# Performance work log

Hardware: AMD Instinct MI355X
Metric: run time of the kernel (lower is better)

The kernel has to match this reference:

```python
import jax, jax.numpy as jnp
from jax import lax
import numpy as np

B, DIM, H, W = 1, 48, 192, 192
HEADS, K, DIL = 2, 7, 3
HD = DIM // HEADS
HID = int(DIM * 2.66)  # 127 (Restormer GEGLU hidden)
EPS = 1e-5


def _window_starts(L, Kk, D):
    # NATTEN window-start rule: keep phase i % D, shift window inside bounds.
    s = np.zeros(L, dtype=np.int32)
    for i in range(L):
        if D <= 1:
            st = max(i - Kk // 2, 0)
            if i + Kk // 2 >= L:
                st = L - Kk
        else:
            st = i - (Kk // 2) * D
            if st < 0:
                st = i % D
            elif i + (Kk // 2) * D >= L:
                imodd = i % D
                a = (L // D) * D
                b = L - a
                if imodd < b:
                    st = L - b + imodd - 2 * (Kk // 2) * D
                else:
                    st = a + imodd - Kk * D
        s[i] = st
    return s


def _nbr_tables(L, Kk, D):
    st = _window_starts(L, Kk, D)
    idx = st[:, None] + np.arange(Kk)[None, :] * D          # [L, K] absolute neighbor idx
    pb = (st - np.arange(L)) // D                            # signed offset of window start (in dilation units)
    pb = pb[:, None] + (Kk - 1) + np.arange(Kk)[None, :]     # [L, K] rpb index in [0, 2K-2]
    return jnp.asarray(idx), jnp.asarray(pb)

IH, PBH = _nbr_tables(H, K, DIL)
IW, PBW = _nbr_tables(W, K, DIL)


def layernorm(x, w, b):  # channel LN on NCHW (WithBias, biased var)
    mu = x.mean(1, keepdims=True)
    var = ((x - mu) ** 2).mean(1, keepdims=True)
    return (x - mu) / jnp.sqrt(var + EPS) * w[None, :, None, None] + b[None, :, None, None]


def na2d(x, qkv_w, qkv_b, rpb, proj_w, proj_b):
    # x: NCHW -> BHWC
    t = x.transpose(0, 2, 3, 1)
    qkv = t @ qkv_w.T + qkv_b                                # [B,H,W,3*DIM]
    qkv = qkv.reshape(B, H, W, 3, HEADS, HD)
    q, k, v = qkv[:, :, :, 0], qkv[:, :, :, 1], qkv[:, :, :, 2]
    q = q * (HD ** -0.5)
    # gather dilated 7x7 neighborhoods: [B, H, K, W, K, heads, hd]
    kn = k[:, IH[:, :, None, None], IW[None, None, :, :]]
    vn = v[:, IH[:, :, None, None], IW[None, None, :, :]]
    attn = jnp.einsum('bijnc,bixjync->bijnxy', q, kn)        # [B,H,W,heads,K,K]
    bias = rpb[:, PBH][:, :, :, PBW]                         # [heads,H,K,W,K]
    attn = attn + bias.transpose(1, 3, 0, 2, 4)
    attn = jax.nn.softmax(attn.reshape(B, H, W, HEADS, K * K), axis=-1)
    attn = attn.reshape(B, H, W, HEADS, K, K)
    out = jnp.einsum('bijnxy,bixjync->bijnc', attn, vn).reshape(B, H, W, DIM)
    out = out @ proj_w.T + proj_b
    return out.transpose(0, 3, 1, 2)


def chan_mod(x, eca_w):  # ECA-style gate: GAP -> 1D conv over channels -> sigmoid
    p = x.mean((2, 3))                                       # [B,C]
    y = lax.conv_general_dilated(p[:, None, :], eca_w[None, None, :], (1,), [(3, 3)],
                                 dimension_numbers=('NCH', 'OIH', 'NCH'))[:, 0, :]
    return jax.nn.sigmoid(y)[:, :, None, None]


def ffn(x, w_in, w_dw, w_out):  # conv-GEGLU
    t = jnp.einsum('bchw,oc->bohw', x, w_in)                 # 1x1: DIM -> 2*HID
    t = lax.conv_general_dilated(t, w_dw, (1, 1), [(1, 1), (1, 1)],
                                 feature_group_count=2 * HID,
                                 dimension_numbers=('NCHW', 'OIHW', 'NCHW'))
    x1, x2 = t[:, :HID], t[:, HID:]
    g = jax.nn.gelu(x1, approximate=False) * x2
    return jnp.einsum('bchw,oc->bohw', g, w_out)             # 1x1: HID -> DIM


def setup_inputs() -> dict:
    key = jax.random.key(0)
    ks = jax.random.split(key, 10)
    d = {
        'x': jax.random.normal(ks[0], (B, DIM, H, W), jnp.float32),
        'ln1_w': jnp.ones((DIM,), jnp.float32),
        'ln1_b': jnp.zeros((DIM,), jnp.float32),
        'qkv_w': jax.random.normal(ks[1], (3 * DIM, DIM), jnp.float32) * 0.05,
        'qkv_b': jnp.zeros((3 * DIM,), jnp.float32),
        'rpb': jax.random.normal(ks[2], (HEADS, 2 * K - 1, 2 * K - 1), jnp.float32) * 0.02,
        'proj_w': jax.random.normal(ks[3], (DIM, DIM), jnp.float32) * 0.05,
        'proj_b': jnp.zeros((DIM,), jnp.float32),
        'eca_w': jax.random.normal(ks[4], (7,), jnp.float32) * 0.1,
        'ln2_w': jnp.ones((DIM,), jnp.float32),
        'ln2_b': jnp.zeros((DIM,), jnp.float32),
        'w_in': jax.random.normal(ks[5], (2 * HID, DIM), jnp.float32) * 0.05,
        'w_dw': jax.random.normal(ks[6], (2 * HID, 1, 3, 3), jnp.float32) * 0.05,
        'w_out': jax.random.normal(ks[7], (DIM, HID), jnp.float32) * 0.05,
    }
    return d


def reference(x, ln1_w, ln1_b, qkv_w, qkv_b, rpb, proj_w, proj_b, eca_w,
              ln2_w, ln2_b, w_in, w_dw, w_out):
    xn1 = layernorm(x, ln1_w, ln1_b)
    x = x + na2d(xn1, qkv_w, qkv_b, rpb, proj_w, proj_b) * chan_mod(xn1, eca_w)
    x = x + ffn(layernorm(x, ln2_w, ln2_b), w_in, w_dw, w_out)
    return x
```

## Files before the change

kernel.cpp:

```cpp
#include <hip/hip_runtime.h>
#include <hip/hip_bf16.h>
#include <math.h>

#define HW_ (192*192)
#define Wd 192
#define HIDc 127
#define NBLK1 (HW_/64)

#define O_LN1W 0
#define O_QKVW 96
#define O_QKVB 7008
#define O_RPB  7152
#define O_PROJW 7490
#define O_PROJB 9794
#define O_ECA  9842
#define O_LN2W 9849
#define O_WIN  9945
#define O_WDW  22137
#define O_WOUT 24423
#define WTS_LEN 30519

typedef unsigned short ushort_t;

__device__ __forceinline__ float b2f(__hip_bfloat16 v){ return __bfloat162float(v); }
__device__ __forceinline__ float u2f(ushort_t h){ return __uint_as_float(((unsigned)h)<<16); }
__device__ __forceinline__ ushort_t f2u(float f){
    __hip_bfloat16 h = __float2bfloat16(f);
    union { __hip_bfloat16 b; ushort_t u; } c; c.b = h; return c.u;
}
__device__ __forceinline__ void up2(unsigned u, float& a, float& b){
    a = __uint_as_float(u << 16);
    b = __uint_as_float(u & 0xffff0000u);
}

__device__ __forceinline__ int wstart(int i){
    if (i < 9) return i % 3;
    if (i >= 183) return 171 + (i % 3);
    return i - 9;
}

__global__ void convert_kernel(
    const void* p0, const void* p1, const void* p2, const void* p3,
    const void* p4, const void* p5, const void* p6, const void* p7,
    const void* p8, const void* p9, const void* p10, const void* p11,
    const void* p12, const ushort_t* __restrict__ xu, int* __restrict__ mode_out,
    float* __restrict__ wts, ushort_t* __restrict__ qkvbf, float* __restrict__ woutT)
{
    __shared__ int sbad;
    if (threadIdx.x == 0) sbad = 0;
    __syncthreads();
    {
        unsigned u = xu[2*threadIdx.x];
        float f = __uint_as_float(u << 16);
        if (!(fabsf(f) < 100.f)) atomicAdd(&sbad, 1);
    }
    __syncthreads();
    const int md = (sbad > 16) ? 1 : 0;
    if (blockIdx.x == 0 && threadIdx.x == 0) mode_out[0] = md;

    const void* ps[13] = {p0,p1,p2,p3,p4,p5,p6,p7,p8,p9,p10,p11,p12};
    const int sz[13]  = {48,48,6912,144,338,2304,48,7,48,48,12192,2286,6096};
    const int off[13] = {O_LN1W,48,O_QKVW,O_QKVB,O_RPB,O_PROJW,O_PROJB,O_ECA,
                         O_LN2W,9897,O_WIN,O_WDW,O_WOUT};
    int b = blockIdx.x;
    if (b == 13){
        if (md){
            const float* s = (const float*)p2;
            for (int i = threadIdx.x; i < 6912; i += 256) qkvbf[i] = f2u(s[i]);
        } else {
            const ushort_t* s = (const ushort_t*)p2;
            for (int i = threadIdx.x; i < 6912; i += 256) qkvbf[i] = s[i];
        }
        return;
    }
    if (b == 14){
        if (md){
            const float* s = (const float*)p12;
            for (int i = threadIdx.x; i < 6096; i += 256){
                int c = i / 48, o = i - c*48;
                woutT[i] = s[o*127 + c];
            }
        } else {
            const __hip_bfloat16* s = (const __hip_bfloat16*)p12;
            for (int i = threadIdx.x; i < 6096; i += 256){
                int c = i / 48, o = i - c*48;
                woutT[i] = b2f(s[o*127 + c]);
            }
        }
        return;
    }
    int n = sz[b];
    float* dst = wts + off[b];
    if (md){
        const float* s = (const float*)ps[b];
        for (int i = threadIdx.x; i < n; i += 256) dst[i] = s[i];
    } else {
        const __hip_bfloat16* s = (const __hip_bfloat16*)ps[b];
        for (int i = threadIdx.x; i < n; i += 256) dst[i] = b2f(s[i]);
    }
}

__global__ __launch_bounds__(384) void ln1qkv_kernel(
    const void* __restrict__ x, const int* __restrict__ mode,
    const float* __restrict__ wts, const ushort_t* __restrict__ qkvbf,
    ushort_t* __restrict__ q, ushort_t* __restrict__ k, ushort_t* __restrict__ v,
    float* __restrict__ chpart)
{
    __shared__ float sx[64*49];

    const int tid  = threadIdx.x;
    const int px_l = tid & 63;
    const int r6   = __builtin_amdgcn_readfirstlane(tid >> 6);
    const int p0   = blockIdx.x * 64;
    const int p    = p0 + px_l;

    if (mode[0]){
        const float* xf = (const float*)x;
        for (int idx = tid; idx < 64*48; idx += 384){
            int c = idx >> 6, pl = idx & 63;
            sx[pl*49 + c] = xf[c*HW_ + p0 + pl];
        }
    } else {
        const __hip_bfloat16* xb = (const __hip_bfloat16*)x;
        for (int idx = tid; idx < 64*48; idx += 384){
            int c = idx >> 6, pl = idx & 63;
            sx[pl*49 + c] = b2f(xb[c*HW_ + p0 + pl]);
        }
    }
    __syncthreads();

    float xr[48];
    float mu = 0.f;
    #pragma unroll
    for (int c = 0; c < 48; c++){ xr[c] = sx[px_l*49 + c]; mu += xr[c]; }
    mu *= (1.f/48.f);
    float var = 0.f;
    #pragma unroll
    for (int c = 0; c < 48; c++){ float d = xr[c]-mu; var += d*d; }
    var *= (1.f/48.f);
    float rs = rsqrtf(var + 1e-5f);
    #pragma unroll
    for (int c = 0; c < 48; c++)
        xr[c] = (xr[c]-mu)*rs*wts[O_LN1W + c] + wts[O_LN1W + 48 + c];

    if (tid < 64){
        #pragma unroll
        for (int c = 0; c < 48; c++){
            float s = xr[c];
            s += __shfl_xor(s, 1);  s += __shfl_xor(s, 2);  s += __shfl_xor(s, 4);
            s += __shfl_xor(s, 8);  s += __shfl_xor(s, 16); s += __shfl_xor(s, 32);
            if (tid == 0) chpart[blockIdx.x*48 + c] = s;
        }
    }

    const int rbase = r6 * 24;
    const float scale = (r6 < 2) ? 0.20412414523193154f : 1.0f;
    float ov[24];
    #pragma unroll 4
    for (int ro = 0; ro < 24; ro++){
        int r = rbase + ro;
        float acc = wts[O_QKVB + r];
        const uint4* wr = (const uint4*)(qkvbf + r*48);
        #pragma unroll
        for (int c8 = 0; c8 < 6; c8++){
            uint4 u = wr[c8];
            float f0,f1,f2,f3,f4,f5,f6,f7;
            up2(u.x,f0,f1); up2(u.y,f2,f3); up2(u.z,f4,f5); up2(u.w,f6,f7);
            acc += f0*xr[8*c8]   + f1*xr[8*c8+1] + f2*xr[8*c8+2] + f3*xr[8*c8+3]
                 + f4*xr[8*c8+4] + f5*xr[8*c8+5] + f6*xr[8*c8+6] + f7*xr[8*c8+7];
        }
        ov[ro] = acc * scale;
    }

    unsigned int pk[12];
    #pragma unroll
    for (int d = 0; d < 12; d++)
        pk[d] = (unsigned)f2u(ov[2*d]) | ((unsigned)f2u(ov[2*d+1]) << 16);
    ushort_t* tp = (r6 >> 1) == 0 ? q : ((r6 >> 1) == 1 ? k : v);
    uint4* dst4 = (uint4*)(tp + (size_t)p*48 + (r6 & 1)*24);
    dst4[0] = make_uint4(pk[0], pk[1], pk[2],  pk[3]);
    dst4[1] = make_uint4(pk[4], pk[5], pk[6],  pk[7]);
    dst4[2] = make_uint4(pk[8], pk[9], pk[10], pk[11]);
}

__global__ __launch_bounds__(256) void gatered_kernel(
    const float* __restrict__ chpart, float* __restrict__ msum)
{
    __shared__ float red[4];
    const int c = blockIdx.x;
    const int tid = threadIdx.x;
    float acc = 0.f;
    for (int b = tid; b < NBLK1; b += 256)
        acc += chpart[b*48 + c];
    acc += __shfl_xor(acc, 1);  acc += __shfl_xor(acc, 2);  acc += __shfl_xor(acc, 4);
    acc += __shfl_xor(acc, 8);  acc += __shfl_xor(acc, 16); acc += __shfl_xor(acc, 32);
    if ((tid & 63) == 0) red[tid >> 6] = acc;
    __syncthreads();
    if (tid == 0)
        msum[c] = (red[0] + red[1] + red[2] + red[3]) * (1.f / (float)HW_);
}

__global__ void gate_kernel(const float* __restrict__ msum,
                            const float* __restrict__ wts,
                            float* __restrict__ gate)
{
    __shared__ float m[48];
    int t = threadIdx.x;
    if (t < 48) m[t] = msum[t];
    __syncthreads();
    if (t < 48){
        float a = 0.f;
        for (int kk = 0; kk < 7; kk++){
            int cc = t + kk - 3;
            if (cc >= 0 && cc < 48) a += wts[O_ECA + kk] * m[cc];
        }
        gate[t] = 1.f / (1.f + expf(-a));
    }
}

__global__ __launch_bounds__(256) void attn_kernel(
    const ushort_t* __restrict__ q, const ushort_t* __restrict__ k,
    const ushort_t* __restrict__ v, const float* __restrict__ wts,
    ushort_t* __restrict__ aout)
{
    const int head = blockIdx.y;
    __shared__ float srpb[169];
    for (int i = threadIdx.x; i < 169; i += 256) srpb[i] = wts[O_RPB + head*169 + i];
    __syncthreads();

    const int tid  = threadIdx.x;
    const int px   = blockIdx.x * 128 + (tid >> 1);
    const int half = tid & 1;
    const int i = px / Wd, j = px % Wd;
    const int sti = wstart(i), stj = wstart(j);
    const int pbi = (sti - i) / 3 + 6;
    const int pbj = (stj - j) / 3 + 6;
    const int choff = head*24 + half*12;

    float qr[12];
    {
        const ushort4* qp = (const ushort4*)(q + (size_t)px*48 + choff);
        #pragma unroll
        for (int b = 0; b < 3; b++){
            ushort4 uu = qp[b];
            qr[4*b]   = u2f(uu.x); qr[4*b+1] = u2f(uu.y);
            qr[4*b+2] = u2f(uu.z); qr[4*b+3] = u2f(uu.w);
        }
    }

    float m = -1e30f, s = 0.f;
    float acc[12];
    #pragma unroll
    for (int c = 0; c < 12; c++) acc[c] = 0.f;

    #pragma unroll
    for (int xx = 0; xx < 7; xx++){
        int ii = sti + 3*xx;
        #pragma unroll
        for (int yy = 0; yy < 7; yy++){
            int jj = stj + 3*yy;
            const size_t nb = (size_t)(ii*Wd + jj)*48 + choff;
            const ushort4* kp = (const ushort4*)(k + nb);
            const ushort4* vp = (const ushort4*)(v + nb);
            ushort4 k0 = kp[0], k1 = kp[1], k2 = kp[2];
            ushort4 v0 = vp[0], v1 = vp[1], v2 = vp[2];
            float d = qr[0]*u2f(k0.x) + qr[1]*u2f(k0.y)
                    + qr[2]*u2f(k0.z) + qr[3]*u2f(k0.w)
                    + qr[4]*u2f(k1.x) + qr[5]*u2f(k1.y)
                    + qr[6]*u2f(k1.z) + qr[7]*u2f(k1.w)
                    + qr[8]*u2f(k2.x) + qr[9]*u2f(k2.y)
                    + qr[10]*u2f(k2.z) + qr[11]*u2f(k2.w);
            d += __shfl_xor(d, 1);
            float sc = d + srpb[(pbi+xx)*13 + (pbj+yy)];
            float mn = fmaxf(m, sc);
            float corr = __expf(m - mn);
            float p = __expf(sc - mn);
            s = s*corr + p;
            m = mn;
            acc[0]  = acc[0] *corr + p*u2f(v0.x);
            acc[1]  = acc[1] *corr + p*u2f(v0.y);
            acc[2]  = acc[2] *corr + p*u2f(v0.z);
            acc[3]  = acc[3] *corr + p*u2f(v0.w);
            acc[4]  = acc[4] *corr + p*u2f(v1.x);
            acc[5]  = acc[5] *corr + p*u2f(v1.y);
            acc[6]  = acc[6] *corr + p*u2f(v1.z);
            acc[7]  = acc[7] *corr + p*u2f(v1.w);
            acc[8]  = acc[8] *corr + p*u2f(v2.x);
            acc[9]  = acc[9] *corr + p*u2f(v2.y);
            acc[10] = acc[10]*corr + p*u2f(v2.z);
            acc[11] = acc[11]*corr + p*u2f(v2.w);
        }
    }
    const float inv = 1.f / s;
    #pragma unroll
    for (int c = 0; c < 12; c++)
        aout[(size_t)(choff + c)*HW_ + px] = f2u(acc[c] * inv);
}

__global__ __launch_bounds__(512) void projpw1_kernel(
    const ushort_t* __restrict__ aout, const float* __restrict__ wts,
    const float* __restrict__ gate, const void* __restrict__ x,
    const int* __restrict__ mode, float* __restrict__ x2,
    ushort_t* __restrict__ t)
{
    __shared__ float saout[64*49];
    __shared__ float sx2[64*49];

    const int tid  = threadIdx.x;
    const int px_l = tid & 63;
    const int og   = __builtin_amdgcn_readfirstlane(tid >> 6);
    const int px0  = blockIdx.x * 64;
    const int px   = px0 + px_l;

    for (int idx = tid; idx < 64*48; idx += 512){
        int c = idx >> 6, pl = idx & 63;
        saout[pl*49 + c] = u2f(aout[(size_t)c*HW_ + px0 + pl]);
    }
    __syncthreads();

    float ar[48];
    #pragma unroll
    for (int c = 0; c < 48; c++) ar[c] = saout[px_l*49 + c];

    const float* xf = (const float*)x;
    const __hip_bfloat16* xb = (const __hip_bfloat16*)x;
    const int md = mode[0];
    const int ob = og * 6;
    #pragma unroll
    for (int oo = 0; oo < 6; oo++){
        int o = ob + oo;
        float acc = wts[O_PROJB + o];
        const float4* swr = (const float4*)&wts[O_PROJW + o*48];
        #pragma unroll
        for (int c4 = 0; c4 < 12; c4++){
            float4 w = swr[c4];
            acc += w.x*ar[4*c4] + w.y*ar[4*c4+1] + w.z*ar[4*c4+2] + w.w*ar[4*c4+3];
        }
        float res = md ? xf[o*HW_ + px] : b2f(xb[o*HW_ + px]);
        float val = res + acc * gate[o];
        x2[o*HW_ + px] = val;
        sx2[px_l*49 + o] = val;
    }
    __syncthreads();

    float xr[48];
    float mu = 0.f;
    #pragma unroll
    for (int c = 0; c < 48; c++){ xr[c] = sx2[px_l*49 + c]; mu += xr[c]; }
    mu *= (1.f/48.f);
    float var = 0.f;
    #pragma unroll
    for (int c = 0; c < 48; c++){ float d = xr[c]-mu; var += d*d; }
    var *= (1.f/48.f);
    float rs = rsqrtf(var + 1e-5f);
    #pragma unroll
    for (int c = 0; c < 48; c++)
        xr[c] = (xr[c]-mu)*rs*wts[O_LN2W + c] + wts[O_LN2W + 48 + c];

    const int o20 = og * 32;
    #pragma unroll 2
    for (int t2 = 0; t2 < 32; t2++){
        int o2 = o20 + t2;
        if (o2 >= 254) break;
        float acc = 0.f;
        const float4* swr = (const float4*)&wts[O_WIN + o2*48];
        #pragma unroll
        for (int c4 = 0; c4 < 12; c4++){
            float4 w = swr[c4];
            acc += w.x*xr[4*c4] + w.y*xr[4*c4+1] + w.z*xr[4*c4+2] + w.w*xr[4*c4+3];
        }
        t[(size_t)o2*HW_ + px] = f2u(acc);
    }
}

__global__ __launch_bounds__(256) void dw_kernel(
    const ushort_t* __restrict__ t, const float* __restrict__ wts,
    ushort_t* __restrict__ g)
{
    int ch = blockIdx.y;
    int p  = blockIdx.x * 256 + threadIdx.x;
    int i  = p / Wd, j = p % Wd;
    float w1[9], w2[9];
    #pragma unroll
    for (int s = 0; s < 9; s++){
        w1[s] = wts[O_WDW + ch*9 + s];
        w2[s] = wts[O_WDW + (ch+HIDc)*9 + s];
    }
    const ushort_t* t1 = t + (size_t)ch * HW_;
    const ushort_t* t2 = t + (size_t)(ch+HIDc) * HW_;
    float a1 = 0.f, a2 = 0.f;
    #pragma unroll
    for (int di = 0; di < 3; di++){
        int ii = i + di - 1;
        if (ii < 0 || ii >= 192) continue;
        #pragma unroll
        for (int dj = 0; dj < 3; dj++){
            int jj = j + dj - 1;
            if (jj < 0 || jj >= 192) continue;
            int off = ii*Wd + jj;
            a1 += w1[di*3+dj]*u2f(t1[off]);
            a2 += w2[di*3+dj]*u2f(t2[off]);
        }
    }
    float ge = a1 * 0.5f * (1.f + erff(a1 * 0.70710678118654752f));
    g[(size_t)ch*HW_ + p] = f2u(ge * a2);
}

__global__ __launch_bounds__(128) void pw2_kernel(
    const ushort_t* __restrict__ g, const float* __restrict__ woutT,
    const float* __restrict__ x2, void* __restrict__ outv,
    const int* __restrict__ mode)
{
    const int ob = blockIdx.y * 12;
    const int p  = blockIdx.x * 128 + threadIdx.x;
    float acc[12];
    #pragma unroll
    for (int o = 0; o < 12; o++) acc[o] = 0.f;
    #pragma unroll 4
    for (int c = 0; c < 127; c++){
        float gv = u2f(g[(size_t)c*HW_ + p]);
        const float* wr = woutT + c*48 + ob;
        #pragma unroll
        for (int o = 0; o < 12; o++) acc[o] += wr[o]*gv;
    }
    if (mode[0]){
        float* out = (float*)outv;
        #pragma unroll
        for (int o = 0; o < 12; o++){
            int oc = ob + o;
            out[(size_t)oc*HW_ + p] = x2[(size_t)oc*HW_ + p] + acc[o];
        }
    } else {
        __hip_bfloat16* out = (__hip_bfloat16*)outv;
        #pragma unroll
        for (int o = 0; o < 12; o++){
            int oc = ob + o;
            out[(size_t)oc*HW_ + p] =
                __float2bfloat16(x2[(size_t)oc*HW_ + p] + acc[o]);
        }
    }
}

extern "C" void kernel_launch(void* const* d_in, const int* in_sizes, int n_in,
                              void* d_out, int out_size, void* d_ws, size_t ws_size,
                              hipStream_t stream)
{
    (void)in_sizes; (void)n_in; (void)out_size;

    char* ws = (char*)d_ws;
    ushort_t* q    = (ushort_t*)(ws);
    ushort_t* k    = (ushort_t*)(ws + 3538944);
    ushort_t* v    = (ushort_t*)(ws + 7077888);
    ushort_t* aout = (ushort_t*)(ws + 10616832);
    ushort_t* t    = (ushort_t*)(ws);
    float*    x2   = (float*)   (ws + 18726912);
    ushort_t* g    = (ushort_t*)(ws + 25804800);
    float*    gate = (float*)   (ws + 35168448);
    int*      mode = (int*)     (ws + 35168640);
    float*    wts  = (float*)   (ws + 35168656);
    float*    chpart=(float*)   (ws + 35168656 + (size_t)WTS_LEN*4);
    float*    msum = chpart + (size_t)NBLK1*48;
    ushort_t* qkvbf= (ushort_t*)(msum + 48);
    float*    woutT= (float*)(qkvbf + 6912);

    size_t need = 35168656 + (size_t)WTS_LEN*4 + (size_t)NBLK1*48*4 + 48*4
                + 6912*2 + 6096*4;
    if (ws_size < need) return;

    convert_kernel<<<15, 256, 0, stream>>>(
        d_in[1], d_in[2], d_in[3], d_in[4], d_in[5], d_in[6], d_in[7],
        d_in[8], d_in[9], d_in[10], d_in[11], d_in[12], d_in[13],
        (const ushort_t*)d_in[0], mode, wts, qkvbf, woutT);

    ln1qkv_kernel<<<dim3(NBLK1), 384, 0, stream>>>(d_in[0], mode, wts, qkvbf,
                                                   q, k, v, chpart);
    gatered_kernel<<<48, 256, 0, stream>>>(chpart, msum);
    gate_kernel<<<1, 64, 0, stream>>>(msum, wts, gate);
    attn_kernel<<<dim3(HW_/128, 2), 256, 0, stream>>>(q, k, v, wts, aout);
    projpw1_kernel<<<dim3(HW_/64), 512, 0, stream>>>(aout, wts, gate, d_in[0],
                                                     mode, x2, t);
    dw_kernel<<<dim3(HW_/256, 127), 256, 0, stream>>>(t, wts, g);
    pw2_kernel<<<dim3(HW_/128, 4), 128, 0, stream>>>(g, woutT, x2, d_out, mode);
}
```

Baseline: 279.9 us.

## Use bf16 proj/w_in weights and halve projpw1 block size with more outputs per thread

The convert kernel now also produces bf16 copies of the projection and GEGLU input weights. projpw1 reads them with 16-byte packed loads, and each thread now computes 12 proj outputs and 64 pw1 outputs, two rows at a time. The block shrinks from 512 to 256 threads and the shared-memory transpose of aout is dropped in favour of direct coalesced per-channel loads. The aim is fewer weight-load instructions and less LDS traffic, at the cost of more serial work per thread and lower weight precision.

```diff
diff --git a/kernel.cpp b/kernel.cpp
--- a/kernel.cpp
+++ b/kernel.cpp
@@ -39,12 +39,26 @@
     return i - 9;
 }
 
+__device__ __forceinline__ float dot48bf(const uint4* wr, const float* xr){
+    float acc = 0.f;
+    #pragma unroll
+    for (int c8 = 0; c8 < 6; c8++){
+        uint4 u = wr[c8];
+        float f0,f1,f2,f3,f4,f5,f6,f7;
+        up2(u.x,f0,f1); up2(u.y,f2,f3); up2(u.z,f4,f5); up2(u.w,f6,f7);
+        acc += f0*xr[8*c8]   + f1*xr[8*c8+1] + f2*xr[8*c8+2] + f3*xr[8*c8+3]
+             + f4*xr[8*c8+4] + f5*xr[8*c8+5] + f6*xr[8*c8+6] + f7*xr[8*c8+7];
+    }
+    return acc;
+}
+
 __global__ void convert_kernel(
     const void* p0, const void* p1, const void* p2, const void* p3,
     const void* p4, const void* p5, const void* p6, const void* p7,
     const void* p8, const void* p9, const void* p10, const void* p11,
     const void* p12, const ushort_t* __restrict__ xu, int* __restrict__ mode_out,
-    float* __restrict__ wts, ushort_t* __restrict__ qkvbf, float* __restrict__ woutT)
+    float* __restrict__ wts, ushort_t* __restrict__ qkvbf, float* __restrict__ woutT,
+    ushort_t* __restrict__ winbf, ushort_t* __restrict__ projbf)
 {
     __shared__ int sbad;
     if (threadIdx.x == 0) sbad = 0;
@@ -63,28 +77,44 @@
     const int off[13] = {O_LN1W,48,O_QKVW,O_QKVB,O_RPB,O_PROJW,O_PROJB,O_ECA,
                          O_LN2W,9897,O_WIN,O_WDW,O_WOUT};
     int b = blockIdx.x;
-    if (b == 13){
-        if (md){
-            const float* s = (const float*)p2;
-            for (int i = threadIdx.x; i < 6912; i += 256) qkvbf[i] = f2u(s[i]);
-        } else {
-            const ushort_t* s = (const ushort_t*)p2;
-            for (int i = threadIdx.x; i < 6912; i += 256) qkvbf[i] = s[i];
-        }
-        return;
-    }
-    if (b == 14){
-        if (md){
-            const float* s = (const float*)p12;
-            for (int i = threadIdx.x; i < 6096; i += 256){
-                int c = i / 48, o = i - c*48;
-                woutT[i] = s[o*127 + c];
+    if (b >= 13){
+        if (b == 13){
+            if (md){
+                const float* s = (const float*)p2;
+                for (int i = threadIdx.x; i < 6912; i += 256) qkvbf[i] = f2u(s[i]);
+            } else {
+                const ushort_t* s = (const ushort_t*)p2;
+                for (int i = threadIdx.x; i < 6912; i += 256) qkvbf[i] = s[i];
+            }
+        } else if (b == 14){
+            if (md){
+                const float* s = (const float*)p12;
+                for (int i = threadIdx.x; i < 6096; i += 256){
+                    int c = i / 48, o = i - c*48;
+                    woutT[i] = s[o*127 + c];
+                }
+            } else {
+                const __hip_bfloat16* s = (const __hip_bfloat16*)p12;
+                for (int i = threadIdx.x; i < 6096; i += 256){
+                    int c = i / 48, o = i - c*48;
+                    woutT[i] = b2f(s[o*127 + c]);
+                }
+            }
+        } else if (b == 15){
+            if (md){
+                const float* s = (const float*)p10;
+                for (int i = threadIdx.x; i < 12192; i += 256) winbf[i] = f2u(s[i]);
+            } else {
+                const ushort_t* s = (const ushort_t*)p10;
+                for (int i = threadIdx.x; i < 12192; i += 256) winbf[i] = s[i];
             }
         } else {
-            const __hip_bfloat16* s = (const __hip_bfloat16*)p12;
-            for (int i = threadIdx.x; i < 6096; i += 256){
-                int c = i / 48, o = i - c*48;
-                woutT[i] = b2f(s[o*127 + c]);
+            if (md){
+                const float* s = (const float*)p5;
+                for (int i = threadIdx.x; i < 2304; i += 256) projbf[i] = f2u(s[i]);
+            } else {
+                const ushort_t* s = (const ushort_t*)p5;
+                for (int i = threadIdx.x; i < 2304; i += 256) projbf[i] = s[i];
             }
         }
         return;
@@ -159,16 +189,8 @@
     #pragma unroll 4
     for (int ro = 0; ro < 24; ro++){
         int r = rbase + ro;
-        float acc = wts[O_QKVB + r];
-        const uint4* wr = (const uint4*)(qkvbf + r*48);
-        #pragma unroll
-        for (int c8 = 0; c8 < 6; c8++){
-            uint4 u = wr[c8];
-            float f0,f1,f2,f3,f4,f5,f6,f7;
-            up2(u.x,f0,f1); up2(u.y,f2,f3); up2(u.z,f4,f5); up2(u.w,f6,f7);
-            acc += f0*xr[8*c8]   + f1*xr[8*c8+1] + f2*xr[8*c8+2] + f3*xr[8*c8+3]
-                 + f4*xr[8*c8+4] + f5*xr[8*c8+5] + f6*xr[8*c8+6] + f7*xr[8*c8+7];
-        }
+        float acc = wts[O_QKVB + r]
+                  + dot48bf((const uint4*)(qkvbf + r*48), xr);
         ov[ro] = acc * scale;
     }
 
@@ -297,13 +319,13 @@
         aout[(size_t)(choff + c)*HW_ + px] = f2u(acc[c] * inv);
 }
 
-__global__ __launch_bounds__(512) void projpw1_kernel(
+__global__ __launch_bounds__(256) void projpw1_kernel(
     const ushort_t* __restrict__ aout, const float* __restrict__ wts,
+    const ushort_t* __restrict__ projbf, const ushort_t* __restrict__ winbf,
     const float* __restrict__ gate, const void* __restrict__ x,
     const int* __restrict__ mode, float* __restrict__ x2,
     ushort_t* __restrict__ t)
 {
-    __shared__ float saout[64*49];
     __shared__ float sx2[64*49];
 
     const int tid  = threadIdx.x;
@@ -312,30 +334,19 @@
     const int px0  = blockIdx.x * 64;
     const int px   = px0 + px_l;
 
-    for (int idx = tid; idx < 64*48; idx += 512){
-        int c = idx >> 6, pl = idx & 63;
-        saout[pl*49 + c] = u2f(aout[(size_t)c*HW_ + px0 + pl]);
-    }
-    __syncthreads();
-
     float ar[48];
     #pragma unroll
-    for (int c = 0; c < 48; c++) ar[c] = saout[px_l*49 + c];
+    for (int c = 0; c < 48; c++) ar[c] = u2f(aout[(size_t)c*HW_ + px]);
 
     const float* xf = (const float*)x;
     const __hip_bfloat16* xb = (const __hip_bfloat16*)x;
     const int md = mode[0];
-    const int ob = og * 6;
-    #pragma unroll
-    for (int oo = 0; oo < 6; oo++){
+    const int ob = og * 12;
+    #pragma unroll 2
+    for (int oo = 0; oo < 12; oo++){
         int o = ob + oo;
-        float acc = wts[O_PROJB + o];
-        const float4* swr = (const float4*)&wts[O_PROJW + o*48];
-        #pragma unroll
-        for (int c4 = 0; c4 < 12; c4++){
-            float4 w = swr[c4];
-            acc += w.x*ar[4*c4] + w.y*ar[4*c4+1] + w.z*ar[4*c4+2] + w.w*ar[4*c4+3];
-        }
+        float acc = wts[O_PROJB + o]
+                  + dot48bf((const uint4*)(projbf + o*48), ar);
         float res = md ? xf[o*HW_ + px] : b2f(xb[o*HW_ + px]);
         float val = res + acc * gate[o];
         x2[o*HW_ + px] = val;
@@ -357,19 +368,27 @@
     for (int c = 0; c < 48; c++)
         xr[c] = (xr[c]-mu)*rs*wts[O_LN2W + c] + wts[O_LN2W + 48 + c];
 
-    const int o20 = og * 32;
-    #pragma unroll 2
-    for (int t2 = 0; t2 < 32; t2++){
-        int o2 = o20 + t2;
-        if (o2 >= 254) break;
-        float acc = 0.f;
-        const float4* swr = (const float4*)&wts[O_WIN + o2*48];
-        #pragma unroll
-        for (int c4 = 0; c4 < 12; c4++){
-            float4 w = swr[c4];
-            acc += w.x*xr[4*c4] + w.y*xr[4*c4+1] + w.z*xr[4*c4+2] + w.w*xr[4*c4+3];
-        }
-        t[(size_t)o2*HW_ + px] = f2u(acc);
+    const int o20 = og * 64;
+    for (int t2 = 0; t2 < 64; t2 += 2){
+        int oA = o20 + t2;
+        if (oA >= 254) break;
+        const uint4* wA = (const uint4*)(winbf + oA*48);
+        const uint4* wB = (const uint4*)(winbf + (oA+1)*48);
+        float accA = 0.f, accB = 0.f;
+        #pragma unroll
+        for (int c8 = 0; c8 < 6; c8++){
+            uint4 ua = wA[c8];
+            uint4 ub = wB[c8];
+            float a0,a1,a2,a3,a4,a5,a6,a7, b0,b1,b2,b3,b4,b5,b6,b7;
+            up2(ua.x,a0,a1); up2(ua.y,a2,a3); up2(ua.z,a4,a5); up2(ua.w,a6,a7);
+            up2(ub.x,b0,b1); up2(ub.y,b2,b3); up2(ub.z,b4,b5); up2(ub.w,b6,b7);
+            accA += a0*xr[8*c8]   + a1*xr[8*c8+1] + a2*xr[8*c8+2] + a3*xr[8*c8+3]
+                  + a4*xr[8*c8+4] + a5*xr[8*c8+5] + a6*xr[8*c8+6] + a7*xr[8*c8+7];
+            accB += b0*xr[8*c8]   + b1*xr[8*c8+1] + b2*xr[8*c8+2] + b3*xr[8*c8+3]
+                  + b4*xr[8*c8+4] + b5*xr[8*c8+5] + b6*xr[8*c8+6] + b7*xr[8*c8+7];
+        }
+        t[(size_t)oA*HW_ + px]     = f2u(accA);
+        t[(size_t)(oA+1)*HW_ + px] = f2u(accB);
     }
 }
 
@@ -462,23 +481,25 @@
     float*    msum = chpart + (size_t)NBLK1*48;
     ushort_t* qkvbf= (ushort_t*)(msum + 48);
     float*    woutT= (float*)(qkvbf + 6912);
+    ushort_t* winbf= (ushort_t*)(woutT + 6096);
+    ushort_t* projbf=(ushort_t*)(winbf + 12192);
 
     size_t need = 35168656 + (size_t)WTS_LEN*4 + (size_t)NBLK1*48*4 + 48*4
-                + 6912*2 + 6096*4;
+                + 6912*2 + 6096*4 + 12192*2 + 2304*2;
     if (ws_size < need) return;
 
-    convert_kernel<<<15, 256, 0, stream>>>(
+    convert_kernel<<<17, 256, 0, stream>>>(
         d_in[1], d_in[2], d_in[3], d_in[4], d_in[5], d_in[6], d_in[7],
         d_in[8], d_in[9], d_in[10], d_in[11], d_in[12], d_in[13],
-        (const ushort_t*)d_in[0], mode, wts, qkvbf, woutT);
+        (const ushort_t*)d_in[0], mode, wts, qkvbf, woutT, winbf, projbf);
 
     ln1qkv_kernel<<<dim3(NBLK1), 384, 0, stream>>>(d_in[0], mode, wts, qkvbf,
                                                    q, k, v, chpart);
     gatered_kernel<<<48, 256, 0, stream>>>(chpart, msum);
     gate_kernel<<<1, 64, 0, stream>>>(msum, wts, gate);
     attn_kernel<<<dim3(HW_/128, 2), 256, 0, stream>>>(q, k, v, wts, aout);
-    projpw1_kernel<<<dim3(HW_/64), 512, 0, stream>>>(aout, wts, gate, d_in[0],
-                                                     mode, x2, t);
+    projpw1_kernel<<<dim3(HW_/64), 256, 0, stream>>>(aout, wts, projbf, winbf,
+                                                     gate, d_in[0], mode, x2, t);
     dw_kernel<<<dim3(HW_/256, 127), 256, 0, stream>>>(t, wts, g);
     pw2_kernel<<<dim3(HW_/128, 4), 128, 0, stream>>>(g, woutT, x2, d_out, mode);
 }
```

Measured after the change: 267.3 us. 4.5% less time.
